# Optimization experiments

Measured on AMD Instinct MI355X. Metric: run time of the kernel, lower is better.

## Reference

```python
import jax, jax.numpy as jnp
import numpy as np

B, L1, L2, H = 16, 1024, 1024, 768

def setup_inputs() -> dict:
    key = jax.random.key(0)
    k1, k2, k3, k4, k5, k6 = jax.random.split(key, 6)
    x1 = jax.random.normal(k1, (B, L1, H), dtype=jnp.float32)
    x2 = jax.random.normal(k2, (B, L2, H), dtype=jnp.float32)
    # True = padded position (masked out), matching torch masked_fill_ semantics
    x1_mask = jax.random.randint(k3, (B, L1), 0, 2) == 1
    x2_mask = jax.random.randint(k4, (B, L2), 0, 2) == 1
    # shared nn.Linear(H, H) used for both x and y projections
    W = jax.random.normal(k5, (H, H), dtype=jnp.float32) / np.sqrt(H)
    b = jax.random.normal(k6, (H,), dtype=jnp.float32) * 0.01
    return {"x1": x1, "x2": x2, "x1_mask": x1_mask, "x2_mask": x2_mask, "W": W, "b": b}

def reference(x1, x2, x1_mask, x2_mask, W, b):
    # SeqAttnMatch('relu_FC', normalize='sumY') with z = y = x2
    x_proj = jax.nn.relu(jnp.einsum('bid,hd->bih', x1, W) + b)   # [B,L1,H]
    y_proj = jax.nn.relu(jnp.einsum('bjd,hd->bjh', x2, W) + b)   # [B,L2,H]
    scores = jnp.einsum('bih,bjh->bij', x_proj, y_proj)          # [B,L1,L2]
    scores = jnp.where(x2_mask[:, None, :], -jnp.inf, scores)
    alpha = jax.nn.softmax(scores, axis=-1)                      # sum over len2
    att = jnp.einsum('bij,bjd->bid', alpha, x2)                  # [B,L1,H]
    # inter_att_concat = 'concat_dot_diff'
    return jnp.concatenate([x1, att, x1 * att, x1 - att], axis=2)  # [B,L1,4H]
```

## Files before the change

### kernel.cpp

```cpp
#include <hip/hip_runtime.h>


#define B_  16
#define L_  1024
#define H_  768
#define M1_ (B_ * L_)
#define MT_ (2 * M1_)

#define XB_  24576
#define WB_  576
#define TB_  3072

using f32x4  = __attribute__((ext_vector_type(4))) float;
using bf16x8 = __attribute__((ext_vector_type(8))) __bf16;
using u16x8  = __attribute__((ext_vector_type(8))) unsigned short;
using u16x4  = __attribute__((ext_vector_type(4))) unsigned short;

__device__ inline unsigned short f2b(float f) {
  unsigned u = __builtin_bit_cast(unsigned, f);
  u += 0x7FFFu + ((u >> 16) & 1u);
  return (unsigned short)(u >> 16);
}
__device__ inline float b2f(unsigned short u) {
  return __builtin_bit_cast(float, ((unsigned)u) << 16);
}

__device__ inline void gld16(const void* g, void* l) {
  __builtin_amdgcn_global_load_lds(
      (__attribute__((address_space(1))) void*)g,
      (__attribute__((address_space(3))) void*)l, 16, 0, 0);
}

__device__ inline bf16x8 ld_frag_sw(const unsigned short* lds, int row, int quad) {
  const int sl = quad ^ ((row >> 1) & 3);
  u16x8 v = *(const u16x8*)(lds + row * 32 + sl * 8);
  return __builtin_bit_cast(bf16x8, v);
}

#define MFMA(a, b, c) __builtin_amdgcn_mfma_f32_16x16x32_bf16((a), (b), (c), 0, 0, 0)

__global__ __launch_bounds__(256) void k_split(
    const float* __restrict__ x1, const float* __restrict__ x2,
    const float* __restrict__ W,
    unsigned short* __restrict__ Xh, unsigned short* __restrict__ Xl,
    unsigned short* __restrict__ Wh, unsigned short* __restrict__ Wl,
    unsigned short* __restrict__ x2T)
{
  __shared__ unsigned short tile[64][72];
  const int tid = threadIdx.x;
  const int bx  = blockIdx.x;

  if (bx < XB_) {
    const size_t idx = (size_t)bx * 256 + tid;
    const int row = (int)(idx / 192);
    const int col = ((int)(idx % 192)) * 4;
    const float* src = (row < M1_) ? (x1 + (size_t)row * H_ + col)
                                   : (x2 + (size_t)(row - M1_) * H_ + col);
    f32x4 v = *(const f32x4*)src;
    u16x4 h, l;
#pragma unroll
    for (int q = 0; q < 4; ++q) { h[q] = f2b(v[q]); l[q] = f2b(v[q] - b2f(h[q])); }
    *(u16x4*)(Xh + idx * 4) = h;
    *(u16x4*)(Xl + idx * 4) = l;
  } else if (bx < XB_ + WB_) {
    const int idx = (bx - XB_) * 256 + tid;
    f32x4 v = *(const f32x4*)(W + (size_t)idx * 4);
    u16x4 h, l;
#pragma unroll
    for (int q = 0; q < 4; ++q) { h[q] = f2b(v[q]); l[q] = f2b(v[q] - b2f(h[q])); }
    *(u16x4*)(Wh + (size_t)idx * 4) = h;
    *(u16x4*)(Wl + (size_t)idx * 4) = l;
  } else {
    const int t  = bx - (XB_ + WB_);
    const int b  = t / 192;
    const int r  = t % 192;
    const int j0 = (r / 12) * 64;
    const int d0 = (r % 12) * 64;
#pragma unroll
    for (int p = 0; p < 4; ++p) {
      const int idx = tid + p * 256;
      const int jr  = idx >> 4;
      const int dc  = (idx & 15) * 4;
      f32x4 v = *(const f32x4*)(x2 + ((size_t)(b * L_ + j0 + jr)) * H_ + d0 + dc);
#pragma unroll
      for (int q = 0; q < 4; ++q) tile[jr][dc + q] = f2b(v[q]);
    }
    __syncthreads();
#pragma unroll
    for (int p = 0; p < 2; ++p) {
      const int idx = tid + p * 256;
      const int dr  = idx >> 3;
      const int jc  = (idx & 7) * 8;
      u16x8 o;
#pragma unroll
      for (int q = 0; q < 8; ++q) o[q] = tile[jc + q][dr];
      *(u16x8*)(x2T + ((size_t)(b * H_) + d0 + dr) * L_ + j0 + jc) = o;
    }
  }
}

__global__ __launch_bounds__(256) void k_proj(
    const unsigned short* __restrict__ Xh, const unsigned short* __restrict__ Xl,
    const unsigned short* __restrict__ Wh, const unsigned short* __restrict__ Wl,
    const float* __restrict__ bias,
    unsigned short* __restrict__ Ph, unsigned short* __restrict__ Pl)
{
  __shared__ unsigned short Ah[128 * 32];
  __shared__ unsigned short Al[128 * 32];
  __shared__ unsigned short Bh[128 * 32];
  __shared__ unsigned short Bl[128 * 32];

  const int tid  = threadIdx.x;
  const int lane = tid & 63, wv = tid >> 6;
  const int wr = wv >> 1, wc = wv & 1;
  const int quad = lane >> 4, lx = lane & 15;
  const int lr = lane >> 2, ls = lane & 3;
  const int lsw = ls ^ ((lr >> 1) & 3);

  const int n0 = blockIdx.x * 128;
  const int m0 = blockIdx.y * 128;

  f32x4 acc[4][4] = {};

  for (int k0 = 0; k0 < H_; k0 += 32) {
    __syncthreads();
#pragma unroll
    for (int g = 0; g < 2; ++g) {
      const int rowl = wv * 32 + g * 16;
      const int row  = rowl + lr;
      const size_t ga = (size_t)(m0 + row) * H_ + k0 + lsw * 8;
      const size_t gb = (size_t)(n0 + row) * H_ + k0 + lsw * 8;
      gld16(Xh + ga, &Ah[rowl * 32]);
      gld16(Xl + ga, &Al[rowl * 32]);
      gld16(Wh + gb, &Bh[rowl * 32]);
      gld16(Wl + gb, &Bl[rowl * 32]);
    }
    __syncthreads();

    bf16x8 fah[4], fal[4], fbh[4], fbl[4];
#pragma unroll
    for (int t = 0; t < 4; ++t) {
      fah[t] = ld_frag_sw(Ah, wr * 64 + t * 16 + lx, quad);
      fal[t] = ld_frag_sw(Al, wr * 64 + t * 16 + lx, quad);
      fbh[t] = ld_frag_sw(Bh, wc * 64 + t * 16 + lx, quad);
      fbl[t] = ld_frag_sw(Bl, wc * 64 + t * 16 + lx, quad);
    }
#pragma unroll
    for (int i = 0; i < 4; ++i)
#pragma unroll
      for (int j = 0; j < 4; ++j) acc[i][j] = MFMA(fah[i], fbh[j], acc[i][j]);
#pragma unroll
    for (int i = 0; i < 4; ++i)
#pragma unroll
      for (int j = 0; j < 4; ++j) acc[i][j] = MFMA(fah[i], fbl[j], acc[i][j]);
#pragma unroll
    for (int i = 0; i < 4; ++i)
#pragma unroll
      for (int j = 0; j < 4; ++j) acc[i][j] = MFMA(fal[i], fbh[j], acc[i][j]);
  }

#pragma unroll
  for (int j = 0; j < 4; ++j) {
    const int h = n0 + wc * 64 + j * 16 + lx;
    const float bv = bias[h];
#pragma unroll
    for (int i = 0; i < 4; ++i) {
      const int mb = m0 + wr * 64 + i * 16 + quad * 4;
#pragma unroll
      for (int r = 0; r < 4; ++r) {
        float v = acc[i][j][r] + bv;
        v = v > 0.f ? v : 0.f;
        const unsigned short hh = f2b(v);
        const unsigned short ll = f2b(v - b2f(hh));
        const size_t off = (size_t)(mb + r) * H_ + h;
        Ph[off] = hh;
        Pl[off] = ll;
      }
    }
  }
}

__global__ __launch_bounds__(256) void k_scores(
    const unsigned short* __restrict__ Ph, const unsigned short* __restrict__ Pl,
    const int* __restrict__ x2_mask, float* __restrict__ scores)
{
  __shared__ unsigned short Ah[128 * 32];
  __shared__ unsigned short Al[128 * 32];
  __shared__ unsigned short Bh[128 * 32];
  __shared__ unsigned short Bl[128 * 32];

  const int tid  = threadIdx.x;
  const int lane = tid & 63, wv = tid >> 6;
  const int wr = wv >> 1, wc = wv & 1;
  const int quad = lane >> 4, lx = lane & 15;
  const int lr = lane >> 2, ls = lane & 3;
  const int lsw = ls ^ ((lr >> 1) & 3);

  const int j0 = blockIdx.x * 128;
  const int i0 = blockIdx.y * 128;
  const int b  = blockIdx.z;

  f32x4 acc[4][4] = {};

  for (int k0 = 0; k0 < H_; k0 += 32) {
    __syncthreads();
#pragma unroll
    for (int g = 0; g < 2; ++g) {
      const int rowl = wv * 32 + g * 16;
      const int row  = rowl + lr;
      const size_t ga = (size_t)(b * L_ + i0 + row) * H_ + k0 + lsw * 8;
      const size_t gb = (size_t)(M1_ + b * L_ + j0 + row) * H_ + k0 + lsw * 8;
      gld16(Ph + ga, &Ah[rowl * 32]);
      gld16(Pl + ga, &Al[rowl * 32]);
      gld16(Ph + gb, &Bh[rowl * 32]);
      gld16(Pl + gb, &Bl[rowl * 32]);
    }
    __syncthreads();

    bf16x8 fah[4], fal[4], fbh[4], fbl[4];
#pragma unroll
    for (int t = 0; t < 4; ++t) {
      fah[t] = ld_frag_sw(Ah, wr * 64 + t * 16 + lx, quad);
      fal[t] = ld_frag_sw(Al, wr * 64 + t * 16 + lx, quad);
      fbh[t] = ld_frag_sw(Bh, wc * 64 + t * 16 + lx, quad);
      fbl[t] = ld_frag_sw(Bl, wc * 64 + t * 16 + lx, quad);
    }
#pragma unroll
    for (int i = 0; i < 4; ++i)
#pragma unroll
      for (int j = 0; j < 4; ++j) acc[i][j] = MFMA(fah[i], fbh[j], acc[i][j]);
#pragma unroll
    for (int i = 0; i < 4; ++i)
#pragma unroll
      for (int j = 0; j < 4; ++j) acc[i][j] = MFMA(fah[i], fbl[j], acc[i][j]);
#pragma unroll
    for (int i = 0; i < 4; ++i)
#pragma unroll
      for (int j = 0; j < 4; ++j) acc[i][j] = MFMA(fal[i], fbh[j], acc[i][j]);
  }

#pragma unroll
  for (int j = 0; j < 4; ++j) {
    const int jj = j0 + wc * 64 + j * 16 + lx;
    const int mv = x2_mask[b * L_ + jj];
#pragma unroll
    for (int i = 0; i < 4; ++i) {
      const int ib = i0 + wr * 64 + i * 16 + quad * 4;
#pragma unroll
      for (int r = 0; r < 4; ++r) {
        const float v = mv ? -1e30f : acc[i][j][r];
        scores[((size_t)(b * L_) + ib + r) * L_ + jj] = v;
      }
    }
  }
}

__global__ __launch_bounds__(256) void k_softmax(
    const float* __restrict__ scores, unsigned short* __restrict__ alphab)
{
  const size_t row = blockIdx.x;
  const float* p = scores + row * L_;
  const int tid = threadIdx.x;

  f32x4 v = *(const f32x4*)(p + tid * 4);
  float m = fmaxf(fmaxf(v[0], v[1]), fmaxf(v[2], v[3]));
#pragma unroll
  for (int off = 32; off > 0; off >>= 1) m = fmaxf(m, __shfl_down(m, off));

  __shared__ float rmax[4];
  __shared__ float rsum[4];
  const int wid = tid >> 6, lane = tid & 63;
  if (lane == 0) rmax[wid] = m;
  __syncthreads();
  m = fmaxf(fmaxf(rmax[0], rmax[1]), fmaxf(rmax[2], rmax[3]));

  f32x4 e;
#pragma unroll
  for (int q = 0; q < 4; ++q) e[q] = __expf(v[q] - m);
  float s = e[0] + e[1] + e[2] + e[3];
#pragma unroll
  for (int off = 32; off > 0; off >>= 1) s += __shfl_down(s, off);
  if (lane == 0) rsum[wid] = s;
  __syncthreads();
  s = rsum[0] + rsum[1] + rsum[2] + rsum[3];

  const float inv = 1.0f / s;
  u16x4 o;
#pragma unroll
  for (int q = 0; q < 4; ++q) o[q] = f2b(e[q] * inv);
  *(u16x4*)(alphab + row * L_ + tid * 4) = o;
}

__global__ __launch_bounds__(256) void k_att(
    const unsigned short* __restrict__ alphab, const unsigned short* __restrict__ x2T,
    float* __restrict__ att)
{
  __shared__ unsigned short Aa[128 * 32];
  __shared__ unsigned short Bt[128 * 32];

  const int tid  = threadIdx.x;
  const int lane = tid & 63, wv = tid >> 6;
  const int wr = wv >> 1, wc = wv & 1;
  const int quad = lane >> 4, lx = lane & 15;
  const int lr = lane >> 2, ls = lane & 3;
  const int lsw = ls ^ ((lr >> 1) & 3);

  const int d0 = blockIdx.x * 128;
  const int i0 = blockIdx.y * 128;
  const int b  = blockIdx.z;

  f32x4 acc[4][4] = {};

  for (int j0 = 0; j0 < L_; j0 += 32) {
    __syncthreads();
#pragma unroll
    for (int g = 0; g < 2; ++g) {
      const int rowl = wv * 32 + g * 16;
      const int row  = rowl + lr;
      const size_t ga = (size_t)(b * L_ + i0 + row) * L_ + j0 + lsw * 8;
      const size_t gb = ((size_t)(b * H_) + d0 + row) * L_ + j0 + lsw * 8;
      gld16(alphab + ga, &Aa[rowl * 32]);
      gld16(x2T + gb, &Bt[rowl * 32]);
    }
    __syncthreads();

    bf16x8 fa[4], fb[4];
#pragma unroll
    for (int t = 0; t < 4; ++t) {
      fa[t] = ld_frag_sw(Aa, wr * 64 + t * 16 + lx, quad);
      fb[t] = ld_frag_sw(Bt, wc * 64 + t * 16 + lx, quad);
    }
#pragma unroll
    for (int i = 0; i < 4; ++i)
#pragma unroll
      for (int j = 0; j < 4; ++j)
        acc[i][j] = MFMA(fa[i], fb[j], acc[i][j]);
  }

#pragma unroll
  for (int j = 0; j < 4; ++j) {
    const int dd = d0 + wc * 64 + j * 16 + lx;
#pragma unroll
    for (int i = 0; i < 4; ++i) {
      const int ib = i0 + wr * 64 + i * 16 + quad * 4;
#pragma unroll
      for (int r = 0; r < 4; ++r)
        att[((size_t)(b * L_) + ib + r) * H_ + dd] = acc[i][j][r];
    }
  }
}

__global__ __launch_bounds__(256) void k_concat(
    const float* __restrict__ x1, const float* __restrict__ att,
    float* __restrict__ out)
{
  const int gid = blockIdx.x * 256 + threadIdx.x;
  const int row = gid / 192;
  const int c   = (gid % 192) * 4;

  f32x4 xv = *(const f32x4*)(x1  + (size_t)row * H_ + c);
  f32x4 av = *(const f32x4*)(att + (size_t)row * H_ + c);
  f32x4 mv, sv;
#pragma unroll
  for (int q = 0; q < 4; ++q) { mv[q] = xv[q] * av[q]; sv[q] = xv[q] - av[q]; }

  float* ob = out + (size_t)row * (4 * H_) + c;
  *(f32x4*)(ob)          = xv;
  *(f32x4*)(ob + H_)     = av;
  *(f32x4*)(ob + 2 * H_) = mv;
  *(f32x4*)(ob + 3 * H_) = sv;
}

extern "C" void kernel_launch(void* const* d_in, const int* in_sizes, int n_in,
                              void* d_out, int out_size, void* d_ws, size_t ws_size,
                              hipStream_t stream) {
  const float* x1      = (const float*)d_in[0];
  const float* x2      = (const float*)d_in[1];
  const int*   x2_mask = (const int*)d_in[3];
  const float* W       = (const float*)d_in[4];
  const float* bias    = (const float*)d_in[5];
  float* out = (float*)d_out;

  char* o8 = (char*)d_out;
  unsigned short* Ph     = (unsigned short*)o8;
  unsigned short* Pl     = (unsigned short*)(o8 + 50331648);
  float*          scores = (float*)(o8 + 100663296);
  unsigned short* Xh     = (unsigned short*)(o8 + 100663296);
  unsigned short* Wh     = (unsigned short*)(o8 + 167772160);
  unsigned short* Wl     = (unsigned short*)(o8 + 168951808);
  unsigned short* x2T    = (unsigned short*)(o8 + 170131456);
  unsigned short* alphab = (unsigned short*)o8;
  unsigned short* Xl     = (unsigned short*)d_ws;
  float*          att    = (float*)d_ws;

  k_split  <<<dim3(XB_ + WB_ + TB_), 256, 0, stream>>>(x1, x2, W, Xh, Xl, Wh, Wl, x2T);
  k_proj   <<<dim3(6, 256),   256, 0, stream>>>(Xh, Xl, Wh, Wl, bias, Ph, Pl);
  k_scores <<<dim3(8, 8, 16), 256, 0, stream>>>(Ph, Pl, x2_mask, scores);
  k_softmax<<<dim3(16384),    256, 0, stream>>>(scores, alphab);
  k_att    <<<dim3(6, 8, 16), 256, 0, stream>>>(scores ? alphab : alphab, x2T, att);
  k_concat <<<dim3(12288),    256, 0, stream>>>(x1, att, out);
}
```

Measured before the change: 643.7 us.

## Double-buffer 256x256 split-bf16 GEMM tiles with async LDS prefetch and XCD-aware block swizzle

```diff
diff --git a/kernel.cpp b/kernel.cpp
--- a/kernel.cpp
+++ b/kernel.cpp
@@ -38,6 +38,101 @@
 }
 
 #define MFMA(a, b, c) __builtin_amdgcn_mfma_f32_16x16x32_bf16((a), (b), (c), 0, 0, 0)
+
+__device__ __forceinline__ void stage2(const unsigned short* __restrict__ src,
+                                       unsigned short* ldsbase,
+                                       int wv, int lq, int lsw,
+                                       size_t row0, int k0) {
+#pragma unroll
+  for (int g = 0; g < 2; ++g) {
+    const int rowl = wv * 32 + g * 16;
+    gld16(src + (row0 + rowl + lq) * (size_t)H_ + k0 + lsw * 8,
+          ldsbase + rowl * 32);
+  }
+}
+
+__device__ __forceinline__ void gemm3_loop(
+    const unsigned short* __restrict__ Agh, const unsigned short* __restrict__ Agl,
+    const unsigned short* __restrict__ Bgh, const unsigned short* __restrict__ Bgl,
+    size_t arow0, size_t brow0,
+    unsigned short* SA, unsigned short* SB, f32x4 (&acc)[8][4])
+{
+  const int tid  = threadIdx.x;
+  const int lane = tid & 63, wv = tid >> 6;
+  const int wr = wv >> 2, wc = wv & 3;
+  const int quad = lane >> 4, lx = lane & 15;
+  const int lq  = lane >> 2;
+  const int lsw = (lane & 3) ^ ((lane >> 3) & 3);
+  constexpr int HB = 256 * 32;
+
+  stage2(Agh, SA,      wv, lq, lsw, arow0, 0);
+  stage2(Bgh, SB,      wv, lq, lsw, brow0, 0);
+  stage2(Agl, SA + HB, wv, lq, lsw, arow0, 0);
+  stage2(Bgl, SB + HB, wv, lq, lsw, brow0, 0);
+  asm volatile("s_waitcnt vmcnt(4)" ::: "memory");
+  __builtin_amdgcn_s_barrier();
+
+  int c = 0;
+  for (int t = 0; t < H_ / 32; ++t) {
+    unsigned short* sAh = SA + c * (2 * HB);
+    unsigned short* sAl = sAh + HB;
+    unsigned short* sBh = SB + c * (2 * HB);
+    unsigned short* sBl = sBh + HB;
+    unsigned short* dA  = SA + (c ^ 1) * (2 * HB);
+    unsigned short* dB  = SB + (c ^ 1) * (2 * HB);
+    const int  k1   = t * 32 + 32;
+    const bool more = (t < H_ / 32 - 1);
+
+    bf16x8 fah[8], fbh[4];
+#pragma unroll
+    for (int i = 0; i < 8; ++i) fah[i] = ld_frag_sw(sAh, wr * 128 + i * 16 + lx, quad);
+#pragma unroll
+    for (int j = 0; j < 4; ++j) fbh[j] = ld_frag_sw(sBh, wc * 64 + j * 16 + lx, quad);
+    if (more) {
+      stage2(Agh, dA,      wv, lq, lsw, arow0, k1);
+      stage2(Bgh, dB,      wv, lq, lsw, brow0, k1);
+      stage2(Agl, dA + HB, wv, lq, lsw, arow0, k1);
+      stage2(Bgl, dB + HB, wv, lq, lsw, brow0, k1);
+    }
+    __builtin_amdgcn_s_barrier();
+    __builtin_amdgcn_s_setprio(1);
+#pragma unroll
+    for (int i = 0; i < 8; ++i)
+#pragma unroll
+      for (int j = 0; j < 4; ++j) acc[i][j] = MFMA(fah[i], fbh[j], acc[i][j]);
+    __builtin_amdgcn_s_setprio(0);
+    if (more) asm volatile("s_waitcnt vmcnt(8)" ::: "memory");
+    else      asm volatile("s_waitcnt vmcnt(0)" ::: "memory");
+    __builtin_amdgcn_s_barrier();
+
+    bf16x8 fbl[4];
+#pragma unroll
+    for (int j = 0; j < 4; ++j) fbl[j] = ld_frag_sw(sBl, wc * 64 + j * 16 + lx, quad);
+    __builtin_amdgcn_s_barrier();
+    __builtin_amdgcn_s_setprio(1);
+#pragma unroll
+    for (int i = 0; i < 8; ++i)
+#pragma unroll
+      for (int j = 0; j < 4; ++j) acc[i][j] = MFMA(fah[i], fbl[j], acc[i][j]);
+    __builtin_amdgcn_s_setprio(0);
+    __builtin_amdgcn_s_barrier();
+
+    bf16x8 fal[8];
+#pragma unroll
+    for (int i = 0; i < 8; ++i) fal[i] = ld_frag_sw(sAl, wr * 128 + i * 16 + lx, quad);
+    __builtin_amdgcn_s_barrier();
+    __builtin_amdgcn_s_setprio(1);
+#pragma unroll
+    for (int i = 0; i < 8; ++i)
+#pragma unroll
+      for (int j = 0; j < 4; ++j) acc[i][j] = MFMA(fal[i], fbh[j], acc[i][j]);
+    __builtin_amdgcn_s_setprio(0);
+    if (more) asm volatile("s_waitcnt vmcnt(4)" ::: "memory");
+    __builtin_amdgcn_s_barrier();
+
+    c ^= 1;
+  }
+}
 
 __global__ __launch_bounds__(256) void k_split(
     const float* __restrict__ x1, const float* __restrict__ x2,
@@ -99,16 +194,129 @@
   }
 }
 
-__global__ __launch_bounds__(256) void k_proj(
+__global__ __launch_bounds__(512, 2) void k_proj(
     const unsigned short* __restrict__ Xh, const unsigned short* __restrict__ Xl,
     const unsigned short* __restrict__ Wh, const unsigned short* __restrict__ Wl,
     const float* __restrict__ bias,
     unsigned short* __restrict__ Ph, unsigned short* __restrict__ Pl)
 {
-  __shared__ unsigned short Ah[128 * 32];
-  __shared__ unsigned short Al[128 * 32];
-  __shared__ unsigned short Bh[128 * 32];
-  __shared__ unsigned short Bl[128 * 32];
+  __shared__ unsigned short SA[2 * 2 * 256 * 32];
+  __shared__ unsigned short SB[2 * 2 * 256 * 32];
+
+  const int tid  = threadIdx.x;
+  const int lane = tid & 63, wv = tid >> 6;
+  const int wr = wv >> 2, wc = wv & 3;
+  const int quad = lane >> 4, lx = lane & 15;
+
+  const int lin = blockIdx.x;
+  const int s   = (lin & 7) * 48 + (lin >> 3);
+  const int n0  = (s % 3) * 256;
+  const int m0  = (s / 3) * 256;
+
+  f32x4 acc[8][4] = {};
+  gemm3_loop(Xh, Xl, Wh, Wl, (size_t)m0, (size_t)n0, SA, SB, acc);
+
+#pragma unroll
+  for (int j = 0; j < 4; ++j) {
+    const int h = n0 + wc * 64 + j * 16 + lx;
+    const float bv = bias[h];
+#pragma unroll
+    for (int i = 0; i < 8; ++i) {
+      const int mrow = m0 + wr * 128 + i * 16 + quad * 4;
+#pragma unroll
+      for (int r = 0; r < 4; ++r) {
+        float v = acc[i][j][r] + bv;
+        v = v > 0.f ? v : 0.f;
+        const unsigned short hh = f2b(v);
+        const unsigned short ll = f2b(v - b2f(hh));
+        const size_t off = (size_t)(mrow + r) * H_ + h;
+        Ph[off] = hh;
+        Pl[off] = ll;
+      }
+    }
+  }
+}
+
+__global__ __launch_bounds__(512, 2) void k_scores(
+    const unsigned short* __restrict__ Ph, const unsigned short* __restrict__ Pl,
+    const int* __restrict__ x2_mask, float* __restrict__ scores)
+{
+  __shared__ unsigned short SA[2 * 2 * 256 * 32];
+  __shared__ unsigned short SB[2 * 2 * 256 * 32];
+
+  const int tid  = threadIdx.x;
+  const int lane = tid & 63, wv = tid >> 6;
+  const int wr = wv >> 2, wc = wv & 3;
+  const int quad = lane >> 4, lx = lane & 15;
+
+  const int lin = blockIdx.x;
+  const int s   = (lin & 7) * 32 + (lin >> 3);
+  const int j0  = (s & 3) * 256;
+  const int i0  = ((s >> 2) & 3) * 256;
+  const int b   = s >> 4;
+
+  f32x4 acc[8][4] = {};
+  gemm3_loop(Ph, Pl, Ph, Pl,
+             (size_t)(b * L_ + i0), (size_t)(M1_ + b * L_ + j0), SA, SB, acc);
+
+#pragma unroll
+  for (int j = 0; j < 4; ++j) {
+    const int jj = j0 + wc * 64 + j * 16 + lx;
+    const int mv = x2_mask[b * L_ + jj];
+#pragma unroll
+    for (int i = 0; i < 8; ++i) {
+      const int ib = i0 + wr * 128 + i * 16 + quad * 4;
+#pragma unroll
+      for (int r = 0; r < 4; ++r) {
+        const float v = mv ? -1e30f : acc[i][j][r];
+        scores[((size_t)(b * L_) + ib + r) * L_ + jj] = v;
+      }
+    }
+  }
+}
+
+__global__ __launch_bounds__(256) void k_softmax(
+    const float* __restrict__ scores, unsigned short* __restrict__ alphab)
+{
+  const size_t row = blockIdx.x;
+  const float* p = scores + row * L_;
+  const int tid = threadIdx.x;
+
+  f32x4 v = *(const f32x4*)(p + tid * 4);
+  float m = fmaxf(fmaxf(v[0], v[1]), fmaxf(v[2], v[3]));
+#pragma unroll
+  for (int off = 32; off > 0; off >>= 1) m = fmaxf(m, __shfl_down(m, off));
+
+  __shared__ float rmax[4];
+  __shared__ float rsum[4];
+  const int wid = tid >> 6, lane = tid & 63;
+  if (lane == 0) rmax[wid] = m;
+  __syncthreads();
+  m = fmaxf(fmaxf(rmax[0], rmax[1]), fmaxf(rmax[2], rmax[3]));
+
+  f32x4 e;
+#pragma unroll
+  for (int q = 0; q < 4; ++q) e[q] = __expf(v[q] - m);
+  float s = e[0] + e[1] + e[2] + e[3];
+#pragma unroll
+  for (int off = 32; off > 0; off >>= 1) s += __shfl_down(s, off);
+  if (lane == 0) rsum[wid] = s;
+  __syncthreads();
+  s = rsum[0] + rsum[1] + rsum[2] + rsum[3];
+
+  const float inv = 1.0f / s;
+  u16x4 o;
+#pragma unroll
+  for (int q = 0; q < 4; ++q) o[q] = f2b(e[q] * inv);
+  *(u16x4*)(alphab + row * L_ + tid * 4) = o;
+}
+
+__global__ __launch_bounds__(256) void k_att(
+    const unsigned short* __restrict__ alphab, const unsigned short* __restrict__ x2T,
+    float* __restrict__ att)
+{
+  __shared__ unsigned short Aa[128 * 32];
+  __shared__ unsigned short Bt[128 * 32];
 
   const int tid  = threadIdx.x;
   const int lane = tid & 63, wv = tid >> 6;
@@ -117,197 +325,11 @@
   const int lr = lane >> 2, ls = lane & 3;
   const int lsw = ls ^ ((lr >> 1) & 3);
 
-  const int n0 = blockIdx.x * 128;
-  const int m0 = blockIdx.y * 128;
-
-  f32x4 acc[4][4] = {};
-
-  for (int k0 = 0; k0 < H_; k0 += 32) {
-    __syncthreads();
-#pragma unroll
-    for (int g = 0; g < 2; ++g) {
-      const int rowl = wv * 32 + g * 16;
-      const int row  = rowl + lr;
-      const size_t ga = (size_t)(m0 + row) * H_ + k0 + lsw * 8;
-      const size_t gb = (size_t)(n0 + row) * H_ + k0 + lsw * 8;
-      gld16(Xh + ga, &Ah[rowl * 32]);
-      gld16(Xl + ga, &Al[rowl * 32]);
-      gld16(Wh + gb, &Bh[rowl * 32]);
-      gld16(Wl + gb, &Bl[rowl * 32]);
-    }
-    __syncthreads();
-
-    bf16x8 fah[4], fal[4], fbh[4], fbl[4];
-#pragma unroll
-    for (int t = 0; t < 4; ++t) {
-      fah[t] = ld_frag_sw(Ah, wr * 64 + t * 16 + lx, quad);
-      fal[t] = ld_frag_sw(Al, wr * 64 + t * 16 + lx, quad);
-      fbh[t] = ld_frag_sw(Bh, wc * 64 + t * 16 + lx, quad);
-      fbl[t] = ld_frag_sw(Bl, wc * 64 + t * 16 + lx, quad);
-    }
-#pragma unroll
-    for (int i = 0; i < 4; ++i)
-#pragma unroll
-      for (int j = 0; j < 4; ++j) acc[i][j] = MFMA(fah[i], fbh[j], acc[i][j]);
-#pragma unroll
-    for (int i = 0; i < 4; ++i)
-#pragma unroll
-      for (int j = 0; j < 4; ++j) acc[i][j] = MFMA(fah[i], fbl[j], acc[i][j]);
-#pragma unroll
-    for (int i = 0; i < 4; ++i)
-#pragma unroll
-      for (int j = 0; j < 4; ++j) acc[i][j] = MFMA(fal[i], fbh[j], acc[i][j]);
-  }
-
-#pragma unroll
-  for (int j = 0; j < 4; ++j) {
-    const int h = n0 + wc * 64 + j * 16 + lx;
-    const float bv = bias[h];
-#pragma unroll
-    for (int i = 0; i < 4; ++i) {
-      const int mb = m0 + wr * 64 + i * 16 + quad * 4;
-#pragma unroll
-      for (int r = 0; r < 4; ++r) {
-        float v = acc[i][j][r] + bv;
-        v = v > 0.f ? v : 0.f;
-        const unsigned short hh = f2b(v);
-        const unsigned short ll = f2b(v - b2f(hh));
-        const size_t off = (size_t)(mb + r) * H_ + h;
-        Ph[off] = hh;
-        Pl[off] = ll;
-      }
-    }
-  }
-}
-
-__global__ __launch_bounds__(256) void k_scores(
-    const unsigned short* __restrict__ Ph, const unsigned short* __restrict__ Pl,
-    const int* __restrict__ x2_mask, float* __restrict__ scores)
-{
-  __shared__ unsigned short Ah[128 * 32];
-  __shared__ unsigned short Al[128 * 32];
-  __shared__ unsigned short Bh[128 * 32];
-  __shared__ unsigned short Bl[128 * 32];
-
-  const int tid  = threadIdx.x;
-  const int lane = tid & 63, wv = tid >> 6;
-  const int wr = wv >> 1, wc = wv & 1;
-  const int quad = lane >> 4, lx = lane & 15;
-  const int lr = lane >> 2, ls = lane & 3;
-  const int lsw = ls ^ ((lr >> 1) & 3);
-
-  const int j0 = blockIdx.x * 128;
-  const int i0 = blockIdx.y * 128;
-  const int b  = blockIdx.z;
-
-  f32x4 acc[4][4] = {};
-
-  for (int k0 = 0; k0 < H_; k0 += 32) {
-    __syncthreads();
-#pragma unroll
-    for (int g = 0; g < 2; ++g) {
-      const int rowl = wv * 32 + g * 16;
-      const int row  = rowl + lr;
-      const size_t ga = (size_t)(b * L_ + i0 + row) * H_ + k0 + lsw * 8;
-      const size_t gb = (size_t)(M1_ + b * L_ + j0 + row) * H_ + k0 + lsw * 8;
-      gld16(Ph + ga, &Ah[rowl * 32]);
-      gld16(Pl + ga, &Al[rowl * 32]);
-      gld16(Ph + gb, &Bh[rowl * 32]);
-      gld16(Pl + gb, &Bl[rowl * 32]);
-    }
-    __syncthreads();
-
-    bf16x8 fah[4], fal[4], fbh[4], fbl[4];
-#pragma unroll
-    for (int t = 0; t < 4; ++t) {
-      fah[t] = ld_frag_sw(Ah, wr * 64 + t * 16 + lx, quad);
-      fal[t] = ld_frag_sw(Al, wr * 64 + t * 16 + lx, quad);
-      fbh[t] = ld_frag_sw(Bh, wc * 64 + t * 16 + lx, quad);
-      fbl[t] = ld_frag_sw(Bl, wc * 64 + t * 16 + lx, quad);
-    }
-#pragma unroll
-    for (int i = 0; i < 4; ++i)
-#pragma unroll
-      for (int j = 0; j < 4; ++j) acc[i][j] = MFMA(fah[i], fbh[j], acc[i][j]);
-#pragma unroll
-    for (int i = 0; i < 4; ++i)
-#pragma unroll
-      for (int j = 0; j < 4; ++j) acc[i][j] = MFMA(fah[i], fbl[j], acc[i][j]);
-#pragma unroll
-    for (int i = 0; i < 4; ++i)
-#pragma unroll
-      for (int j = 0; j < 4; ++j) acc[i][j] = MFMA(fal[i], fbh[j], acc[i][j]);
-  }
-
-#pragma unroll
-  for (int j = 0; j < 4; ++j) {
-    const int jj = j0 + wc * 64 + j * 16 + lx;
-    const int mv = x2_mask[b * L_ + jj];
-#pragma unroll
-    for (int i = 0; i < 4; ++i) {
-      const int ib = i0 + wr * 64 + i * 16 + quad * 4;
-#pragma unroll
-      for (int r = 0; r < 4; ++r) {
-        const float v = mv ? -1e30f : acc[i][j][r];
-        scores[((size_t)(b * L_) + ib + r) * L_ + jj] = v;
-      }
-    }
-  }
-}
-
-__global__ __launch_bounds__(256) void k_softmax(
-    const float* __restrict__ scores, unsigned short* __restrict__ alphab)
-{
-  const size_t row = blockIdx.x;
-  const float* p = scores + row * L_;
-  const int tid = threadIdx.x;
-
-  f32x4 v = *(const f32x4*)(p + tid * 4);
-  float m = fmaxf(fmaxf(v[0], v[1]), fmaxf(v[2], v[3]));
-#pragma unroll
-  for (int off = 32; off > 0; off >>= 1) m = fmaxf(m, __shfl_down(m, off));
-
-  __shared__ float rmax[4];
-  __shared__ float rsum[4];
-  const int wid = tid >> 6, lane = tid & 63;
-  if (lane == 0) rmax[wid] = m;
-  __syncthreads();
-  m = fmaxf(fmaxf(rmax[0], rmax[1]), fmaxf(rmax[2], rmax[3]));
-
-  f32x4 e;
-#pragma unroll
-  for (int q = 0; q < 4; ++q) e[q] = __expf(v[q] - m);
-  float s = e[0] + e[1] + e[2] + e[3];
-#pragma unroll
-  for (int off = 32; off > 0; off >>= 1) s += __shfl_down(s, off);
-  if (lane == 0) rsum[wid] = s;
-  __syncthreads();
-  s = rsum[0] + rsum[1] + rsum[2] + rsum[3];
-
-  const float inv = 1.0f / s;
-  u16x4 o;
-#pragma unroll
-  for (int q = 0; q < 4; ++q) o[q] = f2b(e[q] * inv);
-  *(u16x4*)(alphab + row * L_ + tid * 4) = o;
-}
-
-__global__ __launch_bounds__(256) void k_att(
-    const unsigned short* __restrict__ alphab, const unsigned short* __restrict__ x2T,
-    float* __restrict__ att)
-{
-  __shared__ unsigned short Aa[128 * 32];
-  __shared__ unsigned short Bt[128 * 32];
-
-  const int tid  = threadIdx.x;
-  const int lane = tid & 63, wv = tid >> 6;
-  const int wr = wv >> 1, wc = wv & 1;
-  const int quad = lane >> 4, lx = lane & 15;
-  const int lr = lane >> 2, ls = lane & 3;
-  const int lsw = ls ^ ((lr >> 1) & 3);
-
-  const int d0 = blockIdx.x * 128;
-  const int i0 = blockIdx.y * 128;
-  const int b  = blockIdx.z;
+  const int lin = blockIdx.x;
+  const int s   = (lin & 7) * 96 + (lin >> 3);
+  const int d0  = (s % 6) * 128;
+  const int i0  = ((s / 6) & 7) * 128;
+  const int b   = s / 48;
 
   f32x4 acc[4][4] = {};
 
@@ -394,9 +416,9 @@
   float*          att    = (float*)d_ws;
 
   k_split  <<<dim3(XB_ + WB_ + TB_), 256, 0, stream>>>(x1, x2, W, Xh, Xl, Wh, Wl, x2T);
-  k_proj   <<<dim3(6, 256),   256, 0, stream>>>(Xh, Xl, Wh, Wl, bias, Ph, Pl);
-  k_scores <<<dim3(8, 8, 16), 256, 0, stream>>>(Ph, Pl, x2_mask, scores);
-  k_softmax<<<dim3(16384),    256, 0, stream>>>(scores, alphab);
-  k_att    <<<dim3(6, 8, 16), 256, 0, stream>>>(scores ? alphab : alphab, x2T, att);
-  k_concat <<<dim3(12288),    256, 0, stream>>>(x1, att, out);
-}
+  k_proj   <<<dim3(384),   512, 0, stream>>>(Xh, Xl, Wh, Wl, bias, Ph, Pl);
+  k_scores <<<dim3(256),   512, 0, stream>>>(Ph, Pl, x2_mask, scores);
+  k_softmax<<<dim3(16384), 256, 0, stream>>>(scores, alphab);
+  k_att    <<<dim3(768),   256, 0, stream>>>(alphab, x2T, att);
+  k_concat <<<dim3(12288), 256, 0, stream>>>(x1, att, out);
+}
```

New measurement: 644.0 us. About the same (+0.0%).
